# Optimization experiments

Measured on AMD Instinct MI355X. Metric: run time of the kernel, lower is better.

The kernel has to match this reference:

```python
import jax, jax.numpy as jnp
import numpy as np
from jax import lax

B, T, D, H, F = 32, 20, 256, 256, 512
C0 = 256  # first deconv channels; fc maps F -> C0*4*4


def setup_inputs() -> dict:
    key = jax.random.key(0)
    ks = iter(jax.random.split(key, 40))
    rn = lambda shape, s=0.05: jax.random.normal(next(ks), shape, jnp.float32) * s
    return dict(
        z=jax.random.normal(next(ks), (B, D), jnp.float32),
        # LSTMDecoder params
        fc_hidden_w=rn((H, D)), fc_hidden_b=jnp.zeros((H,), jnp.float32),
        fc_cell_w=rn((H, D)), fc_cell_b=jnp.zeros((H,), jnp.float32),
        w_ih=rn((4 * H, H)), b_ih=jnp.zeros((4 * H,), jnp.float32),
        w_hh=rn((4 * H, H)), b_hh=jnp.zeros((4 * H,), jnp.float32),
        init_inp=rn((H,)),
        fc_out_w=rn((F, H)), fc_out_b=jnp.zeros((F,), jnp.float32),
        # CNNDecoder params
        cnn_fc_w=rn((C0 * 16, F)), cnn_fc_b=jnp.zeros((C0 * 16,), jnp.float32),
        dw0=rn((256, 128, 4, 4)), g0=jnp.ones((128,), jnp.float32), be0=jnp.zeros((128,), jnp.float32),
        dw1=rn((128, 64, 4, 4)), g1=jnp.ones((64,), jnp.float32), be1=jnp.zeros((64,), jnp.float32),
        dw2=rn((64, 32, 4, 4)), g2=jnp.ones((32,), jnp.float32), be2=jnp.zeros((32,), jnp.float32),
        fw=rn((32, 1, 4, 4)), fb=jnp.zeros((1,), jnp.float32),
    )


def _leaky(x):
    return jnp.where(x > 0, x, 0.2 * x)


def _conv_t(x, w):
    # PyTorch ConvTranspose2d(k=4, s=2, p=1): conv with lhs_dilation=2, pad=k-1-p=2
    return lax.conv_general_dilated(
        x, jnp.flip(w, (2, 3)), window_strides=(1, 1),
        padding=[(2, 2), (2, 2)], lhs_dilation=(2, 2),
        dimension_numbers=('NCHW', 'IOHW', 'NCHW'))


def _bn(x, g, b):
    # BatchNorm2d in training mode: batch statistics over (N, H, W)
    m = x.mean((0, 2, 3), keepdims=True)
    v = x.var((0, 2, 3), keepdims=True)
    return (x - m) * lax.rsqrt(v + 1e-5) * g[None, :, None, None] + b[None, :, None, None]


def reference(z, fc_hidden_w, fc_hidden_b, fc_cell_w, fc_cell_b,
              w_ih, b_ih, w_hh, b_hh, init_inp, fc_out_w, fc_out_b,
              cnn_fc_w, cnn_fc_b, dw0, g0, be0, dw1, g1, be1, dw2, g2, be2, fw, fb):
    bsz = z.shape[0]
    h0 = z @ fc_hidden_w.T + fc_hidden_b
    c0 = z @ fc_cell_w.T + fc_cell_b
    x0 = jnp.broadcast_to(init_inp, (bsz, H))

    def step(carry, _):
        h, c, x = carry
        gates = x @ w_ih.T + b_ih + h @ w_hh.T + b_hh
        i, f, g, o = jnp.split(gates, 4, axis=-1)  # PyTorch gate order i,f,g,o
        c_new = jax.nn.sigmoid(f) * c + jax.nn.sigmoid(i) * jnp.tanh(g)
        h_new = jax.nn.sigmoid(o) * jnp.tanh(c_new)
        return (h_new, c_new, h_new), h_new  # output fed back as next input

    _, outs = lax.scan(step, (h0, c0, x0), None, length=T)  # (T, B, H)
    feats = _leaky(jnp.einsum('tbh,fh->tbf', outs, fc_out_w) + fc_out_b)  # (T, B, F)
    feats = feats.transpose(1, 0, 2).reshape(bsz * T, F)

    h = _leaky(feats @ cnn_fc_w.T + cnn_fc_b).reshape(bsz * T, C0, 4, 4)
    h = _leaky(_bn(_conv_t(h, dw0), g0, be0))  # (N,128,8,8)
    h = _leaky(_bn(_conv_t(h, dw1), g1, be1))  # (N,64,16,16)
    h = _leaky(_bn(_conv_t(h, dw2), g2, be2))  # (N,32,32,32)
    out = jax.nn.sigmoid(_conv_t(h, fw) + fb[None, :, None, None])  # (N,1,64,64)
    return out.reshape(bsz, T, 1, 64, 64)
```

## Files before the change

### kernel.cpp

```cpp
#include <hip/hip_runtime.h>
#include <math.h>

#define B_ 32
#define T_ 20
#define H_ 256
#define F_ 512
#define NT_ 640

typedef __attribute__((ext_vector_type(8))) _Float16 half8v;
typedef __attribute__((ext_vector_type(4))) float f32x4;

__device__ __forceinline__ float sigf(float x){ return 1.f/(1.f+__expf(-x)); }
__device__ __forceinline__ float lrelu(float x){ return x>0.f ? x : 0.2f*x; }
__device__ __forceinline__ float dot4(float4 a, float4 b){
  return fmaf(a.x,b.x, fmaf(a.y,b.y, fmaf(a.z,b.z, a.w*b.w)));
}
__device__ __forceinline__ unsigned short f16bits(float x){
  _Float16 h = (_Float16)x;
  union { _Float16 h; unsigned short u; } cv; cv.h = h; return cv.u;
}

__global__ void k_wc(const float* __restrict__ wih, const float* __restrict__ whh,
                     float* __restrict__ Wc){
  int i = blockIdx.x*256 + threadIdx.x;
  float4 a = ((const float4*)wih)[i];
  float4 b = ((const float4*)whh)[i];
  ((float4*)Wc)[i] = make_float4(a.x+b.x, a.y+b.y, a.z+b.z, a.w+b.w);
}

__global__ void k_bias(const float* __restrict__ wih, const float* __restrict__ bih,
                       const float* __restrict__ bhh, const float* __restrict__ init_inp,
                       float* __restrict__ bias0, float* __restrict__ bias1){
  __shared__ __align__(16) float xs[H_];
  int tid = threadIdx.x;
  xs[tid] = init_inp[tid];
  __syncthreads();
  int j = blockIdx.x*256 + tid;
  const float4* wr = (const float4*)(wih + (size_t)j*H_);
  const float4* xx = (const float4*)xs;
  float acc = 0.f;
  #pragma unroll 8
  for(int k=0;k<H_/4;k++) acc += dot4(wr[k], xx[k]);
  float b1 = bih[j] + bhh[j];
  bias1[j] = b1;
  bias0[j] = acc + b1;
}

__global__ void k_rowfc(const float* __restrict__ z, const float* __restrict__ W,
                        const float* __restrict__ bias, float* __restrict__ out){
  __shared__ __align__(16) float zs[H_];
  int b = blockIdx.x, j = threadIdx.x;
  zs[j] = z[b*H_ + j];
  __syncthreads();
  const float4* wr = (const float4*)(W + (size_t)j*H_);
  const float4* zz = (const float4*)zs;
  float acc = bias[j];
  #pragma unroll 8
  for(int k=0;k<H_/4;k++) acc += dot4(wr[k], zz[k]);
  out[b*H_+j] = acc;
}

__global__ void k_lstm(const float* __restrict__ hprev, int hp_stride,
                       float* __restrict__ c,
                       const float* __restrict__ W, const float* __restrict__ bias,
                       float* __restrict__ hout, int ho_stride){
  __shared__ __align__(16) float hs[H_];
  __shared__ float gs[4][64];
  int b = blockIdx.y, jg = blockIdx.x, tid = threadIdx.x;
  hs[tid] = hprev[(size_t)b*hp_stride + tid];
  __syncthreads();
  int g = tid>>6, jj = tid&63;
  int row = g*H_ + jg*64 + jj;
  const float4* wr = (const float4*)(W + (size_t)row*H_);
  const float4* hh = (const float4*)hs;
  float acc = bias[row];
  #pragma unroll 8
  for(int k=0;k<H_/4;k++) acc += dot4(wr[k], hh[k]);
  gs[g][jj] = acc;
  __syncthreads();
  if(tid < 64){
    int j = jg*64 + tid;
    float iv = gs[0][tid], fv = gs[1][tid], gv = gs[2][tid], ov = gs[3][tid];
    int ci = b*H_ + j;
    float cn = sigf(fv)*c[ci] + sigf(iv)*tanhf(gv);
    c[ci] = cn;
    hout[(size_t)b*ho_stride + j] = sigf(ov)*tanhf(cn);
  }
}

__global__ void k_wcvt(const float* __restrict__ w, unsigned short* __restrict__ o, int n8){
  int i = blockIdx.x*256 + threadIdx.x;
  if(i >= n8) return;
  int base = i*8;
  float4 v0 = *(const float4*)(w+base);
  float4 v1 = *(const float4*)(w+base+4);
  unsigned short h[8] = {f16bits(v0.x),f16bits(v0.y),f16bits(v0.z),f16bits(v0.w),
                         f16bits(v1.x),f16bits(v1.y),f16bits(v1.z),f16bits(v1.w)};
  *(uint4*)(o+base) = *(uint4*)h;
}

template<int Kt>
__global__ __launch_bounds__(256) void k_fcmm(const float* __restrict__ A,
    const unsigned short* __restrict__ Wh, const float* __restrict__ bias,
    float* __restrict__ C, int Nt){
  constexpr int NK = Kt/32;
  __shared__ unsigned short at[64*40];
  __shared__ unsigned short bt[128*40];
  const int tid = threadIdx.x;
  const int m0 = blockIdx.x*64, n0 = blockIdx.y*128;
  const int arow = tid>>2, ach = tid&3;
  const float* pa = A + (size_t)(m0+arow)*Kt + ach*8;
  const int brow = tid>>1, bh = tid&1;
  const uint4* pb = (const uint4*)(Wh + (size_t)(n0+brow)*Kt + bh*16);
  float4 a0 = *(const float4*)pa;
  float4 a1 = *(const float4*)(pa+4);
  uint4 b0 = pb[0], b1 = pb[1];

  const int lane = tid&63, wvi = tid>>6;
  const int wm = wvi>>1, wn = wvi&1;
  const int l15 = lane&15, lh = lane>>4;

  f32x4 acc[2][4] = {};
  for(int ks=0; ks<NK; ++ks){
    __syncthreads();
    {
      unsigned short h[8] = {f16bits(a0.x),f16bits(a0.y),f16bits(a0.z),f16bits(a0.w),
                             f16bits(a1.x),f16bits(a1.y),f16bits(a1.z),f16bits(a1.w)};
      *(uint4*)&at[arow*40 + ach*8] = *(uint4*)h;
    }
    *(uint4*)&bt[brow*40 + bh*16    ] = b0;
    *(uint4*)&bt[brow*40 + bh*16 + 8] = b1;
    __syncthreads();
    if(ks+1 < NK){
      a0 = *(const float4*)(pa + (ks+1)*32);
      a1 = *(const float4*)(pa + (ks+1)*32 + 4);
      b0 = pb[(ks+1)*4]; b1 = pb[(ks+1)*4 + 1];
    }
    half8v Af[2], Bf[4];
    #pragma unroll
    for(int a=0;a<2;a++)
      Af[a] = *(const half8v*)&at[(wm*32 + a*16 + l15)*40 + lh*8];
    #pragma unroll
    for(int b=0;b<4;b++)
      Bf[b] = *(const half8v*)&bt[(wn*64 + b*16 + l15)*40 + lh*8];
    #pragma unroll
    for(int a=0;a<2;a++)
      #pragma unroll
      for(int b=0;b<4;b++)
        acc[a][b] = __builtin_amdgcn_mfma_f32_16x16x32_f16(Af[a], Bf[b], acc[a][b], 0, 0, 0);
  }
  #pragma unroll
  for(int b=0;b<4;b++){
    int n = n0 + wn*64 + b*16 + l15;
    float bv = bias[n];
    #pragma unroll
    for(int a=0;a<2;a++){
      #pragma unroll
      for(int r=0;r<4;r++){
        int m = m0 + wm*32 + a*16 + lh*4 + r;
        C[(size_t)m*Nt + n] = lrelu(acc[a][b][r] + bv);
      }
    }
  }
}

template<int IC, int OC>
__global__ void k_wz(const float* __restrict__ w, unsigned short* __restrict__ Wz){
  constexpr int K9 = 9*IC, N4 = 4*OC;
  int i = blockIdx.x*256 + threadIdx.x;
  if(i >= N4*K9) return;
  int n = i / K9; int k = i - n*K9;
  int oc = n>>2, py = (n>>1)&1, px = n&1;
  int dd = k / IC; int ic = k - dd*IC;
  int dy3 = dd/3, dx3 = dd - 3*dy3;
  int ky = py + 3 - 2*dy3, kx = px + 3 - 2*dx3;
  float v = 0.f;
  if(ky>=0 && ky<4 && kx>=0 && kx<4)
    v = w[(((size_t)ic*OC + oc)*4 + ky)*4 + kx];
  Wz[i] = f16bits(v);
}

template<int IC, int OC, int IH, int NL, int RB, int SR, int BM, bool BNIN>
__global__ __launch_bounds__(256) void k_gemmdc(
    const float* __restrict__ in, const unsigned short* __restrict__ Wz,
    float* __restrict__ out, const float* __restrict__ sc, const float* __restrict__ sh,
    float2* __restrict__ scr, int CB)
{
  constexpr int IW = IH, OW = 2*IH;
  constexpr int S  = IH*IW, S4 = 4*S;
  constexpr int K9 = 9*IC;
  constexpr int ICp = IC + 8;
  constexpr int TS = IH/RB;
  constexpr int P  = NL*SR*IW;
  constexpr int NK = K9/32;
  constexpr int BN = 128;
  constexpr int AM = BM/32;
  static_assert(NL*RB*IW == BM, "BM mismatch");

  __shared__ unsigned short linH[P*ICp];
  __shared__ unsigned short bt[BN*32];

  const int tid = threadIdx.x;
  const int bm = blockIdx.x, bn0 = blockIdx.y*BN;
  const int nimg0 = (bm/TS)*NL;
  const int rg = bm % TS;
  const int W0 = (SR==IH) ? 0 : (rg*RB - 1);

  const int pf_n = tid>>1, pf_h = tid&1;
  const uint4* pf_base = (const uint4*)(Wz + (size_t)(bn0+pf_n)*K9 + pf_h*16);
  uint4 breg0, breg1;

  {
    constexpr int NIT = P*(IC/8)/256;
    #pragma unroll
    for(int it=0; it<NIT; ++it){
      int i = tid + it*256;
      int p = i % P; int icb = (i/P)*8;
      int x = p % IW; int t1 = p/IW; int j = t1 % SR; int nl = t1/SR;
      int gr = W0 + j;
      bool ok = (gr>=0) && (gr<IH);
      const float* src = in + ((size_t)(nimg0+nl)*IC + icb)*S + gr*IW + x;
      unsigned short hh[8];
      #pragma unroll
      for(int e=0;e<8;e++){
        float v = ok ? src[(size_t)e*S] : 0.f;
        if(BNIN) v = lrelu(fmaf(v, sc[icb+e], sh[icb+e]));
        hh[e] = f16bits(v);
      }
      *(uint4*)&linH[p*ICp + icb] = *(uint4*)hh;
    }
  }
  breg0 = pf_base[0]; breg1 = pf_base[1];

  const int lane = tid & 63, wvi = tid>>6;
  const int wm = wvi>>1, wn = wvi&1;
  const int l15 = lane & 15, lh = lane>>4;

  int mxA[AM], mylA[AM], nlA[AM];
  #pragma unroll
  for(int a=0;a<AM;a++){
    int r = wm*(BM/2) + a*16 + l15;
    mxA[a] = r % IW; int t = r/IW; mylA[a] = t % RB; nlA[a] = t/RB;
  }

  f32x4 acc[AM][4] = {};

  for(int ks=0; ks<NK; ++ks){
    __syncthreads();
    *(uint4*)&bt[pf_n*32 + pf_h*16    ] = breg0;
    *(uint4*)&bt[pf_n*32 + pf_h*16 + 8] = breg1;
    __syncthreads();
    if(ks+1 < NK){
      breg0 = pf_base[(ks+1)*4];
      breg1 = pf_base[(ks+1)*4 + 1];
    }

    int k0 = ks*32;
    int dd = k0 / IC; int icb = k0 - dd*IC;
    int dy3 = dd/3, dx3 = dd - 3*dy3;

    half8v Af[AM], Bf[4];
    #pragma unroll
    for(int a=0;a<AM;a++){
      int gx = mxA[a] - 1 + dx3;
      bool vx = (gx>=0) && (gx<IW);
      int gxc = gx<0 ? 0 : (gx>IW-1 ? IW-1 : gx);
      int jyc; bool vy;
      if(SR==IH){
        int jy = mylA[a] - 1 + dy3;
        vy = (jy>=0) && (jy<IH);
        jyc = jy<0 ? 0 : (jy>SR-1 ? SR-1 : jy);
      } else {
        jyc = mylA[a] + dy3; vy = true;
      }
      int p = (nlA[a]*SR + jyc)*IW + gxc;
      half8v f = *(const half8v*)&linH[p*ICp + icb + lh*8];
      if(!(vx&&vy)){
        #pragma unroll
        for(int e=0;e<8;e++) f[e] = (_Float16)0.f;
      }
      Af[a] = f;
    }
    #pragma unroll
    for(int b=0;b<4;b++)
      Bf[b] = *(const half8v*)&bt[(wn*64 + b*16 + l15)*32 + lh*8];

    #pragma unroll
    for(int a=0;a<AM;a++)
      #pragma unroll
      for(int b=0;b<4;b++)
        acc[a][b] = __builtin_amdgcn_mfma_f32_16x16x32_f16(Bf[b], Af[a], acc[a][b], 0, 0, 0);
  }

  #pragma unroll
  for(int b=0;b<4;b++){
    float s_ = 0.f, q_ = 0.f;
    int Nbase = bn0 + wn*64 + b*16 + lh*4;
    #pragma unroll
    for(int r=0;r<4;r++){
      int N = Nbase + r;
      int oc = N>>2, py = (N>>1)&1, px = N&1;
      #pragma unroll
      for(int a=0;a<AM;a++){
        float v = acc[a][b][r];
        int myg = (SR==IH) ? mylA[a] : (rg*RB + mylA[a]);
        out[((size_t)(nimg0+nlA[a])*OC + oc)*S4 + (size_t)(2*myg+py)*OW + (2*mxA[a]+px)] = v;
        s_ += v; q_ = fmaf(v,v,q_);
      }
    }
    s_ += __shfl_xor(s_,1); q_ += __shfl_xor(q_,1);
    s_ += __shfl_xor(s_,2); q_ += __shfl_xor(q_,2);
    s_ += __shfl_xor(s_,4); q_ += __shfl_xor(q_,4);
    s_ += __shfl_xor(s_,8); q_ += __shfl_xor(q_,8);
    if(l15 == 0){
      int oc = ((bn0 + wn*64 + b*16)>>2) + lh;
      scr[(size_t)oc*CB + bm*2 + wm] = make_float2(s_, q_);
    }
  }
}

__global__ void k_bnred(const float2* __restrict__ scr, float* __restrict__ sum,
                        float* __restrict__ sq, int CB){
  int oc = blockIdx.x, tid = threadIdx.x;
  float s = 0.f, q = 0.f;
  for(int i = tid; i < CB; i += 256){
    float2 v = scr[(size_t)oc*CB + i];
    s += v.x; q += v.y;
  }
  #pragma unroll
  for(int m=1;m<64;m<<=1){ s += __shfl_xor(s,m); q += __shfl_xor(q,m); }
  __shared__ float ls[4], lq[4];
  int w = tid>>6;
  if((tid&63)==0){ ls[w]=s; lq[w]=q; }
  __syncthreads();
  if(tid==0){
    sum[oc] = ls[0]+ls[1]+ls[2]+ls[3];
    sq[oc]  = lq[0]+lq[1]+lq[2]+lq[3];
  }
}

template<int OC, int SP>
__global__ void k_bn(float* __restrict__ x, const float* __restrict__ ssum,
                     const float* __restrict__ ssq, const float* __restrict__ g,
                     const float* __restrict__ be, int n4){
  int i = blockIdx.x*256 + threadIdx.x;
  if(i >= n4) return;
  int c = ((i*4)/SP) % OC;
  const float inv_cnt = 1.f/(640.f*SP);
  float m = ssum[c]*inv_cnt;
  float var = ssq[c]*inv_cnt - m*m;
  float sc = g[c]*rsqrtf(var + 1e-5f);
  float sh = be[c] - m*sc;
  float4 xv = ((float4*)x)[i];
  xv.x = lrelu(fmaf(xv.x, sc, sh));
  xv.y = lrelu(fmaf(xv.y, sc, sh));
  xv.z = lrelu(fmaf(xv.z, sc, sh));
  xv.w = lrelu(fmaf(xv.w, sc, sh));
  ((float4*)x)[i] = xv;
}

__global__ __launch_bounds__(256,3) void k_final(const float* __restrict__ in,
    const float* __restrict__ w, float* __restrict__ dout, const float* __restrict__ fb){
  constexpr int IC = 32, IH = 32, IW = 32, OW = 64, RB = 8, SR = RB+2;
  __shared__ float lin[IC*SR*IW];
  __shared__ __align__(16) float lw[IC*16];

  int rg = blockIdx.x;
  int n = blockIdx.y;
  int tid = threadIdx.x;

  {
    const float4* src = (const float4*)in;
    float4* dst = (float4*)lin;
    constexpr int NV4 = IC*SR*IW/4;
    #pragma unroll
    for(int i=0;i<NV4/256;i++){
      int idx = tid + i*256;
      int ic = idx/(SR*8); int rem = idx - ic*(SR*8);
      int j = rem/8; int c4 = rem - j*8;
      int gr = RB*rg - 1 + j;
      gr = gr < 0 ? 0 : (gr > IH-1 ? IH-1 : gr);
      dst[idx] = src[((size_t)(n*IC+ic)*IH + gr)*8 + c4];
    }
    if(tid < 128) ((float4*)lw)[tid] = ((const float4*)w)[tid];
  }
  float fbv = fb[0];
  __syncthreads();

  int tl = tid / IW, tx = tid % IW;
  int ty = RB*rg + tl;

  int offs[3][3]; float msk[3][3];
  #pragma unroll
  for(int dy=0;dy<3;dy++){
    int iy = ty-1+dy; bool vy = (iy>=0)&&(iy<IH);
    #pragma unroll
    for(int dx=0;dx<3;dx++){
      int ix = tx-1+dx; bool vx = (ix>=0)&&(ix<IW);
      int lcol = ix < 0 ? 0 : (ix > IW-1 ? IW-1 : ix);
      offs[dy][dx] = (tl+dy)*IW + lcol;
      msk[dy][dx]  = (vy&&vx) ? 1.f : 0.f;
    }
  }

  float acc[2][2] = {{0.f,0.f},{0.f,0.f}};
  #pragma unroll 4
  for(int ic=0; ic<IC; ic++){
    const float* p = lin + ic*(SR*IW);
    float v[3][3];
    #pragma unroll
    for(int dy=0;dy<3;dy++)
      #pragma unroll
      for(int dx=0;dx<3;dx++)
        v[dy][dx] = p[offs[dy][dx]] * msk[dy][dx];
    const float4* wr = (const float4*)(lw + ic*16);
    float4 w0=wr[0], w1=wr[1], w2=wr[2], w3=wr[3];
    float wv[16] = {w0.x,w0.y,w0.z,w0.w, w1.x,w1.y,w1.z,w1.w,
                    w2.x,w2.y,w2.z,w2.w, w3.x,w3.y,w3.z,w3.w};
    #pragma unroll
    for(int r=0;r<2;r++)
      #pragma unroll
      for(int s2=0;s2<2;s2++)
        #pragma unroll
        for(int a=0;a<2;a++)
          #pragma unroll
          for(int b2=0;b2<2;b2++)
            acc[r][s2] = fmaf(v[a+r][b2+s2], wv[(3-2*a-r)*4 + (3-2*b2-s2)], acc[r][s2]);
  }

  float* ob = dout + (size_t)n*OW*OW;
  #pragma unroll
  for(int r=0;r<2;r++)
    #pragma unroll
    for(int s2=0;s2<2;s2++){
      float vv = acc[r][s2] + fbv;
      ob[(2*ty+r)*OW + (2*tx+s2)] = 1.f/(1.f+__expf(-vv));
    }
}

extern "C" void kernel_launch(void* const* d_in, const int* in_sizes, int n_in,
                              void* d_out, int out_size, void* d_ws, size_t ws_size,
                              hipStream_t stream){
  const float* z       = (const float*)d_in[0];
  const float* fhw     = (const float*)d_in[1];
  const float* fhb     = (const float*)d_in[2];
  const float* fcw     = (const float*)d_in[3];
  const float* fcb     = (const float*)d_in[4];
  const float* wih     = (const float*)d_in[5];
  const float* bih     = (const float*)d_in[6];
  const float* whh     = (const float*)d_in[7];
  const float* bhh     = (const float*)d_in[8];
  const float* init_inp= (const float*)d_in[9];
  const float* fow     = (const float*)d_in[10];
  const float* fob     = (const float*)d_in[11];
  const float* cfw     = (const float*)d_in[12];
  const float* cfb     = (const float*)d_in[13];
  const float* dw0     = (const float*)d_in[14];
  const float* g0      = (const float*)d_in[15];
  const float* be0     = (const float*)d_in[16];
  const float* dw1     = (const float*)d_in[17];
  const float* g1      = (const float*)d_in[18];
  const float* be1     = (const float*)d_in[19];
  const float* dw2     = (const float*)d_in[20];
  const float* g2      = (const float*)d_in[21];
  const float* be2     = (const float*)d_in[22];
  const float* fw      = (const float*)d_in[23];
  const float* fb      = (const float*)d_in[24];

  float* ws    = (float*)d_ws;
  float* conv2 = ws;
  float* conv1 = ws + 20971520;
  float* conv0 = ws + 31457280;
  float* fc1   = ws + 36700160;
  float* feats = ws + 39321600;
  float* outs  = ws + 39649280;
  float* Wc    = ws + 39813120;
  float* bias0 = ws + 40075264;
  float* bias1 = ws + 40076288;
  float* h0    = ws + 40077312;
  float* cbuf  = ws + 40085504;
  float* stats = ws + 40093696;
  float* sum0 = stats,     *sq0 = stats+128;
  float* sum1 = stats+256, *sq1 = stats+320;
  float* sum2 = stats+384, *sq2 = stats+416;

  unsigned short* Wz0 = (unsigned short*)conv2;
  unsigned short* Wz1 = (unsigned short*)(conv2 + 600000);
  unsigned short* Whf = (unsigned short*)(conv2 + 1000000);
  unsigned short* Fof = (unsigned short*)(conv2 + 2100000);
  unsigned short* Wz2 = (unsigned short*)feats;
  float2* scr0 = (float2*)outs;
  float2* scr1 = (float2*)(outs + 81920);
  float2* scr2 = (float2*)(feats + 40960);

  hipLaunchKernelGGL(k_wc,    dim3(256), dim3(256), 0, stream, wih, whh, Wc);
  hipLaunchKernelGGL(k_bias,  dim3(4),   dim3(256), 0, stream, wih, bih, bhh, init_inp, bias0, bias1);
  hipLaunchKernelGGL(k_rowfc, dim3(32),  dim3(256), 0, stream, z, fhw, fhb, h0);
  hipLaunchKernelGGL(k_rowfc, dim3(32),  dim3(256), 0, stream, z, fcw, fcb, cbuf);
  hipLaunchKernelGGL(k_wcvt,  dim3(1024), dim3(256), 0, stream, cfw, Whf, 262144);
  hipLaunchKernelGGL(k_wcvt,  dim3(64),   dim3(256), 0, stream, fow, Fof, 16384);

  for(int t=0;t<T_;t++){
    const float* W  = (t==0) ? whh   : Wc;
    const float* bs = (t==0) ? bias0 : bias1;
    const float* hp = (t==0) ? h0    : outs + (t-1)*H_;
    int hps         = (t==0) ? H_    : T_*H_;
    hipLaunchKernelGGL(k_lstm, dim3(4,32), dim3(256), 0, stream,
                       hp, hps, cbuf, W, bs, outs + t*H_, T_*H_);
  }

  hipLaunchKernelGGL((k_fcmm<256>), dim3(10,4), dim3(256), 0, stream, outs, Fof, fob, feats, 512);
  hipLaunchKernelGGL((k_fcmm<512>), dim3(10,32), dim3(256), 0, stream, feats, Whf, cfb, fc1, 4096);

  hipLaunchKernelGGL((k_wz<256,128>), dim3(4608), dim3(256), 0, stream, dw0, Wz0);
  hipLaunchKernelGGL((k_wz<128,64>),  dim3(1152), dim3(256), 0, stream, dw1, Wz1);
  hipLaunchKernelGGL((k_wz<64,32>),   dim3(288),  dim3(256), 0, stream, dw2, Wz2);

  hipLaunchKernelGGL((k_gemmdc<256,128,4,4,4,4,64,false>), dim3(160,4), dim3(256), 0, stream,
                     fc1, Wz0, conv0, (const float*)nullptr, (const float*)nullptr, scr0, 320);
  hipLaunchKernelGGL(k_bnred, dim3(128), dim3(256), 0, stream, scr0, sum0, sq0, 320);
  hipLaunchKernelGGL((k_bn<128,64>),   dim3(5120),  dim3(256), 0, stream, conv0, sum0, sq0, g0, be0, 1310720);

  hipLaunchKernelGGL((k_gemmdc<128,64,8,2,8,8,128,false>), dim3(320,2), dim3(256), 0, stream,
                     conv0, Wz1, conv1, (const float*)nullptr, (const float*)nullptr, scr1, 640);
  hipLaunchKernelGGL(k_bnred, dim3(64), dim3(256), 0, stream, scr1, sum1, sq1, 640);
  hipLaunchKernelGGL((k_bn<64,256>),   dim3(10240), dim3(256), 0, stream, conv1, sum1, sq1, g1, be1, 2621440);

  hipLaunchKernelGGL((k_gemmdc<64,32,16,1,8,10,128,false>), dim3(1280,1), dim3(256), 0, stream,
                     conv1, Wz2, conv2, (const float*)nullptr, (const float*)nullptr, scr2, 2560);
  hipLaunchKernelGGL(k_bnred, dim3(32), dim3(256), 0, stream, scr2, sum2, sq2, 2560);
  hipLaunchKernelGGL((k_bn<32,1024>),  dim3(20480), dim3(256), 0, stream, conv2, sum2, sq2, g2, be2, 5242880);

  hipLaunchKernelGGL(k_final, dim3(4,640), dim3(256), 0, stream, conv2, fw, (float*)d_out, fb);
}
```

Before: 494.3 us.

## Fuse BatchNorm apply into next conv's input load and use fp16 LSTM weights

Removes the standalone BatchNorm+LeakyReLU passes over the three conv outputs. A tiny kernel now computes per-channel scale and shift, and the next deconv GEMM (BNIN=true) or the final conv applies them while loading its input, saving a full read and write of each large activation tensor. The LSTM recurrent weights are also converted to fp16 once and read as half8 vectors, halving weight traffic per step. The cost is some precision loss in the LSTM matvec and extra conversion launches.

Result: faster. 424.9 us (-14.0%).

```diff
diff --git a/kernel.cpp b/kernel.cpp
--- a/kernel.cpp
+++ b/kernel.cpp
@@ -62,7 +62,7 @@
 
 __global__ void k_lstm(const float* __restrict__ hprev, int hp_stride,
                        float* __restrict__ c,
-                       const float* __restrict__ W, const float* __restrict__ bias,
+                       const unsigned short* __restrict__ Wf, const float* __restrict__ bias,
                        float* __restrict__ hout, int ho_stride){
   __shared__ __align__(16) float hs[H_];
   __shared__ float gs[4][64];
@@ -71,11 +71,15 @@
   __syncthreads();
   int g = tid>>6, jj = tid&63;
   int row = g*H_ + jg*64 + jj;
-  const float4* wr = (const float4*)(W + (size_t)row*H_);
-  const float4* hh = (const float4*)hs;
+  const half8v* wr = (const half8v*)(Wf + (size_t)row*H_);
   float acc = bias[row];
   #pragma unroll 8
-  for(int k=0;k<H_/4;k++) acc += dot4(wr[k], hh[k]);
+  for(int k=0;k<H_/8;k++){
+    half8v w8 = wr[k];
+    const float* hp8 = hs + k*8;
+    #pragma unroll
+    for(int e=0;e<8;e++) acc = fmaf((float)w8[e], hp8[e], acc);
+  }
   gs[g][jj] = acc;
   __syncthreads();
   if(tid < 64){
@@ -223,8 +227,11 @@
       unsigned short hh[8];
       #pragma unroll
       for(int e=0;e<8;e++){
-        float v = ok ? src[(size_t)e*S] : 0.f;
-        if(BNIN) v = lrelu(fmaf(v, sc[icb+e], sh[icb+e]));
+        float v = 0.f;
+        if(ok){
+          v = src[(size_t)e*S];
+          if(BNIN) v = lrelu(fmaf(v, sc[icb+e], sh[icb+e]));
+        }
         hh[e] = f16bits(v);
       }
       *(uint4*)&linH[p*ICp + icb] = *(uint4*)hh;
@@ -339,28 +346,22 @@
   }
 }
 
-template<int OC, int SP>
-__global__ void k_bn(float* __restrict__ x, const float* __restrict__ ssum,
-                     const float* __restrict__ ssq, const float* __restrict__ g,
-                     const float* __restrict__ be, int n4){
-  int i = blockIdx.x*256 + threadIdx.x;
-  if(i >= n4) return;
-  int c = ((i*4)/SP) % OC;
-  const float inv_cnt = 1.f/(640.f*SP);
-  float m = ssum[c]*inv_cnt;
-  float var = ssq[c]*inv_cnt - m*m;
-  float sc = g[c]*rsqrtf(var + 1e-5f);
-  float sh = be[c] - m*sc;
-  float4 xv = ((float4*)x)[i];
-  xv.x = lrelu(fmaf(xv.x, sc, sh));
-  xv.y = lrelu(fmaf(xv.y, sc, sh));
-  xv.z = lrelu(fmaf(xv.z, sc, sh));
-  xv.w = lrelu(fmaf(xv.w, sc, sh));
-  ((float4*)x)[i] = xv;
+__global__ void k_bnscale(const float* __restrict__ ssum, const float* __restrict__ ssq,
+                          const float* __restrict__ g, const float* __restrict__ be,
+                          float* __restrict__ sc, float* __restrict__ sh,
+                          int OCn, float inv_cnt){
+  int t = threadIdx.x;
+  if(t < OCn){
+    float m = ssum[t]*inv_cnt;
+    float var = ssq[t]*inv_cnt - m*m;
+    float s = g[t]*rsqrtf(var + 1e-5f);
+    sc[t] = s; sh[t] = be[t] - m*s;
+  }
 }
 
 __global__ __launch_bounds__(256,3) void k_final(const float* __restrict__ in,
-    const float* __restrict__ w, float* __restrict__ dout, const float* __restrict__ fb){
+    const float* __restrict__ w, float* __restrict__ dout, const float* __restrict__ fb,
+    const float* __restrict__ sc, const float* __restrict__ sh){
   constexpr int IC = 32, IH = 32, IW = 32, OW = 64, RB = 8, SR = RB+2;
   __shared__ float lin[IC*SR*IW];
   __shared__ __align__(16) float lw[IC*16];
@@ -380,7 +381,13 @@
       int j = rem/8; int c4 = rem - j*8;
       int gr = RB*rg - 1 + j;
       gr = gr < 0 ? 0 : (gr > IH-1 ? IH-1 : gr);
-      dst[idx] = src[((size_t)(n*IC+ic)*IH + gr)*8 + c4];
+      float4 v = src[((size_t)(n*IC+ic)*IH + gr)*8 + c4];
+      float s = sc[ic], h2 = sh[ic];
+      v.x = lrelu(fmaf(v.x, s, h2));
+      v.y = lrelu(fmaf(v.y, s, h2));
+      v.z = lrelu(fmaf(v.z, s, h2));
+      v.w = lrelu(fmaf(v.w, s, h2));
+      dst[idx] = v;
     }
     if(tid < 128) ((float4*)lw)[tid] = ((const float4*)w)[tid];
   }
@@ -480,15 +487,21 @@
   float* h0    = ws + 40077312;
   float* cbuf  = ws + 40085504;
   float* stats = ws + 40093696;
+  float* scsh  = ws + 40094144;
   float* sum0 = stats,     *sq0 = stats+128;
   float* sum1 = stats+256, *sq1 = stats+320;
   float* sum2 = stats+384, *sq2 = stats+416;
-
-  unsigned short* Wz0 = (unsigned short*)conv2;
-  unsigned short* Wz1 = (unsigned short*)(conv2 + 600000);
-  unsigned short* Whf = (unsigned short*)(conv2 + 1000000);
-  unsigned short* Fof = (unsigned short*)(conv2 + 2100000);
-  unsigned short* Wz2 = (unsigned short*)feats;
+  float* sc0 = scsh,      *sh0 = scsh+128;
+  float* sc1 = scsh+256,  *sh1 = scsh+320;
+  float* sc2 = scsh+384,  *sh2 = scsh+416;
+
+  unsigned short* Wz0   = (unsigned short*)conv2;
+  unsigned short* Wz1   = (unsigned short*)(conv2 + 600000);
+  unsigned short* Whf   = (unsigned short*)(conv2 + 1000000);
+  unsigned short* Fof   = (unsigned short*)(conv2 + 2100000);
+  unsigned short* Wc16  = (unsigned short*)(conv2 + 2200000);
+  unsigned short* Whh16 = (unsigned short*)(conv2 + 2400000);
+  unsigned short* Wz2   = (unsigned short*)feats;
   float2* scr0 = (float2*)outs;
   float2* scr1 = (float2*)(outs + 81920);
   float2* scr2 = (float2*)(feats + 40960);
@@ -499,14 +512,16 @@
   hipLaunchKernelGGL(k_rowfc, dim3(32),  dim3(256), 0, stream, z, fcw, fcb, cbuf);
   hipLaunchKernelGGL(k_wcvt,  dim3(1024), dim3(256), 0, stream, cfw, Whf, 262144);
   hipLaunchKernelGGL(k_wcvt,  dim3(64),   dim3(256), 0, stream, fow, Fof, 16384);
+  hipLaunchKernelGGL(k_wcvt,  dim3(128),  dim3(256), 0, stream, whh, Whh16, 32768);
+  hipLaunchKernelGGL(k_wcvt,  dim3(128),  dim3(256), 0, stream, Wc, Wc16, 32768);
 
   for(int t=0;t<T_;t++){
-    const float* W  = (t==0) ? whh   : Wc;
+    const unsigned short* Wf = (t==0) ? Whh16 : Wc16;
     const float* bs = (t==0) ? bias0 : bias1;
     const float* hp = (t==0) ? h0    : outs + (t-1)*H_;
     int hps         = (t==0) ? H_    : T_*H_;
     hipLaunchKernelGGL(k_lstm, dim3(4,32), dim3(256), 0, stream,
-                       hp, hps, cbuf, W, bs, outs + t*H_, T_*H_);
+                       hp, hps, cbuf, Wf, bs, outs + t*H_, T_*H_);
   }
 
   hipLaunchKernelGGL((k_fcmm<256>), dim3(10,4), dim3(256), 0, stream, outs, Fof, fob, feats, 512);
@@ -518,18 +533,21 @@
 
   hipLaunchKernelGGL((k_gemmdc<256,128,4,4,4,4,64,false>), dim3(160,4), dim3(256), 0, stream,
                      fc1, Wz0, conv0, (const float*)nullptr, (const float*)nullptr, scr0, 320);
-  hipLaunchKernelGGL(k_bnred, dim3(128), dim3(256), 0, stream, scr0, sum0, sq0, 320);
-  hipLaunchKernelGGL((k_bn<128,64>),   dim3(5120),  dim3(256), 0, stream, conv0, sum0, sq0, g0, be0, 1310720);
-
-  hipLaunchKernelGGL((k_gemmdc<128,64,8,2,8,8,128,false>), dim3(320,2), dim3(256), 0, stream,
-                     conv0, Wz1, conv1, (const float*)nullptr, (const float*)nullptr, scr1, 640);
-  hipLaunchKernelGGL(k_bnred, dim3(64), dim3(256), 0, stream, scr1, sum1, sq1, 640);
-  hipLaunchKernelGGL((k_bn<64,256>),   dim3(10240), dim3(256), 0, stream, conv1, sum1, sq1, g1, be1, 2621440);
-
-  hipLaunchKernelGGL((k_gemmdc<64,32,16,1,8,10,128,false>), dim3(1280,1), dim3(256), 0, stream,
-                     conv1, Wz2, conv2, (const float*)nullptr, (const float*)nullptr, scr2, 2560);
-  hipLaunchKernelGGL(k_bnred, dim3(32), dim3(256), 0, stream, scr2, sum2, sq2, 2560);
-  hipLaunchKernelGGL((k_bn<32,1024>),  dim3(20480), dim3(256), 0, stream, conv2, sum2, sq2, g2, be2, 5242880);
-
-  hipLaunchKernelGGL(k_final, dim3(4,640), dim3(256), 0, stream, conv2, fw, (float*)d_out, fb);
-}
+  hipLaunchKernelGGL(k_bnred,  dim3(128), dim3(256), 0, stream, scr0, sum0, sq0, 320);
+  hipLaunchKernelGGL(k_bnscale, dim3(1), dim3(128), 0, stream, sum0, sq0, g0, be0, sc0, sh0,
+                     128, 1.f/(640.f*64.f));
+
+  hipLaunchKernelGGL((k_gemmdc<128,64,8,2,8,8,128,true>), dim3(320,2), dim3(256), 0, stream,
+                     conv0, Wz1, conv1, sc0, sh0, scr1, 640);
+  hipLaunchKernelGGL(k_bnred,  dim3(64), dim3(256), 0, stream, scr1, sum1, sq1, 640);
+  hipLaunchKernelGGL(k_bnscale, dim3(1), dim3(128), 0, stream, sum1, sq1, g1, be1, sc1, sh1,
+                     64, 1.f/(640.f*256.f));
+
+  hipLaunchKernelGGL((k_gemmdc<64,32,16,1,8,10,128,true>), dim3(1280,1), dim3(256), 0, stream,
+                     conv1, Wz2, conv2, sc1, sh1, scr2, 2560);
+  hipLaunchKernelGGL(k_bnred,  dim3(32), dim3(256), 0, stream, scr2, sum2, sq2, 2560);
+  hipLaunchKernelGGL(k_bnscale, dim3(1), dim3(128), 0, stream, sum2, sq2, g2, be2, sc2, sh2,
+                     32, 1.f/(640.f*1024.f));
+
+  hipLaunchKernelGGL(k_final, dim3(4,640), dim3(256), 0, stream, conv2, fw, (float*)d_out, fb, sc2, sh2);
+}
```
